# Kernel tuning notes

Hardware: AMD Instinct MI355X
Metric: run time of the kernel (lower is better)

Reference implementation:

```python
import jax, jax.numpy as jnp
import numpy as np

NUM_HEADS = 8
ROPE_THETA = 10.0


def _axial_angles(height, width, head_dim, theta):
    # frequencies: 1/theta^(arange(0, head_dim, 4)[:head_dim//4] / head_dim)  -> [head_dim//4]
    hd4 = head_dim // 4
    freqs = 1.0 / (theta ** (np.arange(0, head_dim, 4)[:hd4].astype(np.float32) / head_dim))
    t = np.arange(height * width)
    t_x = (t % width).astype(np.float32)
    t_y = (t // width).astype(np.float32)
    ang_x = np.outer(t_x, freqs)  # [n, head_dim//4]
    ang_y = np.outer(t_y, freqs)
    return jnp.asarray(ang_x), jnp.asarray(ang_y)


def _apply_rope(x, cos, sin):
    # x: [b, h, n, half]; cos/sin: [n, half//2]; complex-pair rotation on last dim
    xr = x[..., 0::2]
    xi = x[..., 1::2]
    out_r = xr * cos - xi * sin
    out_i = xr * sin + xi * cos
    return jnp.stack([out_r, out_i], axis=-1).reshape(x.shape)


def setup_inputs() -> dict:
    key = jax.random.key(0)
    ks = jax.random.split(key, 5)
    b, n, c = 4, 16384, 512
    x = jax.random.normal(ks[0], (b, n, c), dtype=jnp.float32)
    w_qkv = jax.random.normal(ks[1], (c, 3 * c), dtype=jnp.float32) * 0.02
    b_qkv = jax.random.normal(ks[2], (3 * c,), dtype=jnp.float32) * 0.02
    w_proj = jax.random.normal(ks[3], (c, c), dtype=jnp.float32) * 0.02
    b_proj = jax.random.normal(ks[4], (c,), dtype=jnp.float32) * 0.02
    return {"x": x, "w_qkv": w_qkv, "b_qkv": b_qkv, "w_proj": w_proj, "b_proj": b_proj,
            "height": 128, "width": 128}


def reference(x, w_qkv, b_qkv, w_proj, b_proj, height, width):
    b, n, c = x.shape
    h = NUM_HEADS
    hd = c // h
    half = hd // 2

    qkv = (x @ w_qkv + b_qkv).reshape(b, n, 3, h, hd).transpose(2, 0, 3, 1, 4)
    q, k, v = qkv[0], qkv[1], qkv[2]  # each [b, h, n, hd]

    ang_x, ang_y = _axial_angles(height, width, hd, ROPE_THETA)
    cx, sx = jnp.cos(ang_x), jnp.sin(ang_x)
    cy, sy = jnp.cos(ang_y), jnp.sin(ang_y)

    q = jnp.concatenate([_apply_rope(q[..., :half], cx, sx),
                         _apply_rope(q[..., half:], cy, sy)], axis=-1)
    k = jnp.concatenate([_apply_rope(k[..., :half], cx, sx),
                         _apply_rope(k[..., half:], cy, sy)], axis=-1)

    # kernel feature map: elu(x) + 1 (positive)
    q = jax.nn.elu(q) + 1.0
    k = jax.nn.elu(k) + 1.0

    # linear attention: O(n d^2)
    kv = jnp.einsum('bhnd,bhne->bhde', k, v)
    out = jnp.einsum('bhnd,bhde->bhne', q, kv)
    z = 1.0 / (jnp.einsum('bhnd,bhd->bhn', q, k.sum(axis=2)) + 1e-6)
    out = out * z[..., None]

    out = out.transpose(0, 2, 1, 3).reshape(b, n, c)
    return out @ w_proj + b_proj
```

## Files before the change

kernel.cpp:

```cpp
#include <hip/hip_runtime.h>
#include <math.h>

#define BATCH 4
#define NTOK  16384
#define CDIM  512
#define NH    8
#define HD    64
#define M_ROWS (BATCH*NTOK)
#define KDIM  512

typedef _Float16 f16;
typedef _Float16 f16x8 __attribute__((ext_vector_type(8)));
typedef _Float16 f16x4 __attribute__((ext_vector_type(4)));
typedef _Float16 f16x2 __attribute__((ext_vector_type(2)));
typedef float    f32x4 __attribute__((ext_vector_type(4)));

__device__ __forceinline__ void load_lds16(const void* g, void* l) {
    __builtin_amdgcn_global_load_lds(
        (const __attribute__((address_space(1))) void*)g,
        (__attribute__((address_space(3))) void*)l, 16, 0, 0);
}

__global__ void rope_tables(float* __restrict__ tab) {
    int tid = threadIdx.x;
    for (int i = 0; i < 32; i++) {
        int idx = tid + i * 256;
        int grp = idx >> 11;
        int rem = idx & 2047;
        int t   = rem >> 4;
        int fi  = rem & 15;
        float freq_f = (float)pow(10.0, -(double)fi / 16.0);
        double ang = (double)t * (double)freq_f;
        tab[idx] = (float)((grp & 1) ? sin(ang) : cos(ang));
    }
}

__global__ void convert_x_f16(const float* __restrict__ in, f16* __restrict__ outp) {
    int i = blockIdx.x * 256 + threadIdx.x;
    float4 a = *(const float4*)&in[(size_t)i * 8];
    float4 b = *(const float4*)&in[(size_t)i * 8 + 4];
    f16x8 o;
    o[0]=(f16)a.x; o[1]=(f16)a.y; o[2]=(f16)a.z; o[3]=(f16)a.w;
    o[4]=(f16)b.x; o[5]=(f16)b.y; o[6]=(f16)b.z; o[7]=(f16)b.w;
    *(f16x8*)&outp[(size_t)i * 8] = o;
}

__global__ void convert_wT(const float* __restrict__ w, f16* __restrict__ wt, int N) {
    int idx = blockIdx.x * 256 + threadIdx.x;
    int n = idx >> 9, k = idx & 511;
    wt[idx] = (f16)w[(size_t)k * N + n];
}

template<int MODE>
__global__ __launch_bounds__(256, 2)
void gemm_f16(const f16* __restrict__ A, const f16* __restrict__ Bt,
              const float* __restrict__ bias,
              float* __restrict__ Co,
              f16* __restrict__ qd, f16* __restrict__ kd, f16* __restrict__ vd,
              const float* __restrict__ tab)
{
    __shared__ f16 As[128 * 32];
    __shared__ f16 Bs[128 * 32];
    const int tid  = threadIdx.x;
    const int lane = tid & 63;
    const int wave = tid >> 6;
    const int wy = wave >> 1, wx = wave & 1;
    const int row0 = blockIdx.y * 128;
    const int col0 = blockIdx.x * 128;
    const int l15 = lane & 15;
    const int l4  = lane >> 4;

    f32x4 acc[4][4];
    #pragma unroll
    for (int mt = 0; mt < 4; mt++)
        #pragma unroll
        for (int nt = 0; nt < 4; nt++)
            acc[mt][nt] = (f32x4){0.f, 0.f, 0.f, 0.f};

    const int pbase = wave * 128;

    for (int k0 = 0; k0 < KDIM; k0 += 32) {
        #pragma unroll
        for (int i = 0; i < 2; i++) {
            int p = pbase + i * 64 + lane;
            int m = p >> 2;
            int j = p & 3;
            load_lds16(&A [(size_t)(row0 + m) * KDIM + k0 + j * 8], &As[(pbase + i * 64) * 8]);
            load_lds16(&Bt[(size_t)(col0 + m) * KDIM + k0 + j * 8], &Bs[(pbase + i * 64) * 8]);
        }
        __syncthreads();

        f16x8 af[4], bf[4];
        #pragma unroll
        for (int t = 0; t < 4; t++) {
            af[t] = *(const f16x8*)&As[(wy * 64 + t * 16 + l15) * 32 + l4 * 8];
            bf[t] = *(const f16x8*)&Bs[(wx * 64 + t * 16 + l15) * 32 + l4 * 8];
        }
        #pragma unroll
        for (int mt = 0; mt < 4; mt++)
            #pragma unroll
            for (int nt = 0; nt < 4; nt++)
                acc[mt][nt] = __builtin_amdgcn_mfma_f32_16x16x32_f16(af[mt], bf[nt], acc[mt][nt], 0, 0, 0);
        __syncthreads();
    }

    if (MODE == 0) {
        #pragma unroll
        for (int nt = 0; nt < 4; nt++) {
            int col = col0 + wx * 64 + nt * 16 + l15;
            float bv = bias[col];
            #pragma unroll
            for (int mt = 0; mt < 4; mt++)
                #pragma unroll
                for (int r = 0; r < 4; r++) {
                    int row = row0 + wy * 64 + mt * 16 + l4 * 4 + r;
                    Co[(size_t)row * CDIM + col] = acc[mt][nt][r] + bv;
                }
        }
    } else {
        const int which = col0 >> 9;
        f16* dst = (which == 0) ? qd : (which == 1) ? kd : vd;
        #pragma unroll
        for (int nt = 0; nt < 4; nt++) {
            int coln = col0 + wx * 64 + nt * 16 + l15;
            int c512 = coln & 511;
            float bv = bias[coln];
            if (which == 2) {
                #pragma unroll
                for (int mt = 0; mt < 4; mt++)
                    #pragma unroll
                    for (int r = 0; r < 4; r++) {
                        int row = row0 + wy * 64 + mt * 16 + l4 * 4 + r;
                        float val = acc[mt][nt][r] + bv;
                        float pv  = __shfl_xor(val, 1, 64);
                        if (!(lane & 1)) {
                            f16x2 pk; pk[0] = (f16)val; pk[1] = (f16)pv;
                            *(f16x2*)&dst[(size_t)row * CDIM + c512] = pk;
                        }
                    }
            } else {
                int ch  = c512 & 63;
                int isy = ch >> 5;
                int fid = (ch & 31) >> 1;
                const float* ct = tab + (isy ? 4096 : 0)    + fid;
                const float* st = tab + (isy ? 6144 : 2048) + fid;
                #pragma unroll
                for (int mt = 0; mt < 4; mt++)
                    #pragma unroll
                    for (int r = 0; r < 4; r++) {
                        int row = row0 + wy * 64 + mt * 16 + l4 * 4 + r;
                        int tok = row & (NTOK - 1);
                        int t   = isy ? (tok >> 7) : (tok & 127);
                        float c = ct[t * 16], s = st[t * 16];
                        float val = acc[mt][nt][r] + bv;
                        float pv  = __shfl_xor(val, 1, 64);
                        float xr = (lane & 1) ? pv  : val;
                        float xi = (lane & 1) ? val : pv;
                        float o_r = xr * c - xi * s;
                        float o_i = xr * s + xi * c;
                        o_r = (o_r > 0.f) ? o_r + 1.f : __expf(o_r);
                        o_i = (o_i > 0.f) ? o_i + 1.f : __expf(o_i);
                        if (!(lane & 1)) {
                            f16x2 pk; pk[0] = (f16)o_r; pk[1] = (f16)o_i;
                            *(f16x2*)&dst[(size_t)row * CDIM + c512] = pk;
                        }
                    }
            }
        }
    }
}

__global__ __launch_bounds__(256, 4)
void kv_kernel(const f16* __restrict__ kk, const f16* __restrict__ vv,
               float* __restrict__ kv, float* __restrict__ ksum)
{
    int bh = blockIdx.x;
    int b = bh >> 3, h = bh & 7;
    int t0 = blockIdx.y * 1024;
    __shared__ float ks[64][64];
    __shared__ float vs[64][64];
    int tid = threadIdx.x;
    int tx = tid & 15;
    int ty = tid >> 4;
    float acc[4][4];
    float ksacc[4];
    #pragma unroll
    for (int r = 0; r < 4; r++) { ksacc[r] = 0.f;
        #pragma unroll
        for (int j = 0; j < 4; j++) acc[r][j] = 0.f; }

    const size_t rowbase = (size_t)b * NTOK;
    for (int tt = t0; tt < t0 + 1024; tt += 64) {
        #pragma unroll
        for (int i = 0; i < 2; i++) {
            int idx = tid + i * 256;
            int tok = idx >> 3;
            int o   = (idx & 7) * 8;
            size_t g = (rowbase + tt + tok) * CDIM + h * HD + o;
            f16x8 k8 = *(const f16x8*)&kk[g];
            f16x8 v8 = *(const f16x8*)&vv[g];
            #pragma unroll
            for (int e = 0; e < 8; e++) { ks[tok][o + e] = (float)k8[e]; vs[tok][o + e] = (float)v8[e]; }
        }
        __syncthreads();
        #pragma unroll 8
        for (int t = 0; t < 64; t++) {
            float4 kd4 = *(const float4*)&ks[t][ty * 4];
            float4 vd4 = *(const float4*)&vs[t][tx * 4];
            float ka[4] = {kd4.x, kd4.y, kd4.z, kd4.w};
            float va[4] = {vd4.x, vd4.y, vd4.z, vd4.w};
            #pragma unroll
            for (int r = 0; r < 4; r++) {
                ksacc[r] += ka[r];
                #pragma unroll
                for (int j = 0; j < 4; j++) acc[r][j] += ka[r] * va[j];
            }
        }
        __syncthreads();
    }
    #pragma unroll
    for (int r = 0; r < 4; r++)
        #pragma unroll
        for (int j = 0; j < 4; j++)
            atomicAdd(&kv[bh * 4096 + (ty * 4 + r) * 64 + tx * 4 + j], acc[r][j]);
    if (tx == 0) {
        #pragma unroll
        for (int r = 0; r < 4; r++) atomicAdd(&ksum[bh * 64 + ty * 4 + r], ksacc[r]);
    }
}

__global__ __launch_bounds__(256, 4)
void attn_kernel(const f16* __restrict__ q, const float* __restrict__ kv,
                 const float* __restrict__ ksum, f16* __restrict__ attnh)
{
    int bh = blockIdx.x;
    int b = bh >> 3, h = bh & 7;
    int rc = blockIdx.y;
    __shared__ float kvs[64][64];
    __shared__ float qs[64][68];
    __shared__ float ksums[64];
    __shared__ float zpart[64][4];
    __shared__ float zs[64];
    int tid = threadIdx.x;
    int tx = tid & 15;
    int ty = tid >> 4;

    #pragma unroll
    for (int i = 0; i < 4; i++) {
        int idx = tid + i * 256;
        *(float4*)&kvs[idx >> 4][(idx & 15) * 4] = *(const float4*)&kv[bh * 4096 + idx * 4];
    }
    if (tid < 64) ksums[tid] = ksum[bh * 64 + tid];

    for (int sub = 0; sub < 4; sub++) {
        int r0 = rc * 256 + sub * 64;
        #pragma unroll
        for (int i = 0; i < 2; i++) {
            int idx = tid + i * 256;
            int rr = idx >> 3;
            int o  = (idx & 7) * 8;
            f16x8 q8 = *(const f16x8*)&q[((size_t)b * NTOK + r0 + rr) * CDIM + h * HD + o];
            #pragma unroll
            for (int e = 0; e < 8; e++) qs[rr][o + e] = (float)q8[e];
        }
        __syncthreads();
        {
            int row = tid & 63, g = tid >> 6;
            float p = 0.f;
            #pragma unroll
            for (int d = 0; d < 16; d++) p += qs[row][g * 16 + d] * ksums[g * 16 + d];
            zpart[row][g] = p;
        }
        __syncthreads();
        if (tid < 64)
            zs[tid] = 1.f / (zpart[tid][0] + zpart[tid][1] + zpart[tid][2] + zpart[tid][3] + 1e-6f);
        __syncthreads();

        float acc[4][4];
        #pragma unroll
        for (int r = 0; r < 4; r++)
            #pragma unroll
            for (int e = 0; e < 4; e++) acc[r][e] = 0.f;

        for (int d = 0; d < 64; d += 4) {
            float qa[4][4], ka[4][4];
            #pragma unroll
            for (int r = 0; r < 4; r++) {
                float4 v4 = *(const float4*)&qs[ty * 4 + r][d];
                qa[r][0]=v4.x; qa[r][1]=v4.y; qa[r][2]=v4.z; qa[r][3]=v4.w;
            }
            #pragma unroll
            for (int j = 0; j < 4; j++) {
                float4 v4 = *(const float4*)&kvs[d + j][tx * 4];
                ka[j][0]=v4.x; ka[j][1]=v4.y; ka[j][2]=v4.z; ka[j][3]=v4.w;
            }
            #pragma unroll
            for (int r = 0; r < 4; r++)
                #pragma unroll
                for (int j = 0; j < 4; j++)
                    #pragma unroll
                    for (int e = 0; e < 4; e++)
                        acc[r][e] += qa[r][j] * ka[j][e];
        }
        #pragma unroll
        for (int r = 0; r < 4; r++) {
            float z = zs[ty * 4 + r];
            f16x4 o4;
            o4[0] = (f16)(acc[r][0] * z); o4[1] = (f16)(acc[r][1] * z);
            o4[2] = (f16)(acc[r][2] * z); o4[3] = (f16)(acc[r][3] * z);
            *(f16x4*)&attnh[((size_t)b * NTOK + r0 + ty * 4 + r) * CDIM + h * HD + tx * 4] = o4;
        }
        __syncthreads();
    }
}

extern "C" void kernel_launch(void* const* d_in, const int* in_sizes, int n_in,
                              void* d_out, int out_size, void* d_ws, size_t ws_size,
                              hipStream_t stream)
{
    const float* x      = (const float*)d_in[0];
    const float* w_qkv  = (const float*)d_in[1];
    const float* b_qkv  = (const float*)d_in[2];
    const float* w_proj = (const float*)d_in[3];
    const float* b_proj = (const float*)d_in[4];
    float* out = (float*)d_out;
    char*  ws  = (char*)d_ws;

    const size_t NCB = (size_t)M_ROWS * CDIM * sizeof(f16);
    f16*   xh   = (f16*)(ws);
    f16*   qh   = (f16*)(ws + NCB * 1);
    f16*   kh   = (f16*)(ws + NCB * 2);
    f16*   vh   = (f16*)(ws + NCB * 3);
    f16*   wqt  = (f16*)(ws + NCB * 4);
    f16*   wpt  = (f16*)(ws + NCB * 4 + (1536 * 512) * sizeof(f16));
    float* tab  = (float*)(ws + NCB * 4 + (1536 * 512 + 512 * 512) * sizeof(f16));
    float* kvp  = tab + 8192;
    float* ksum = kvp + 32 * 4096;

    hipMemsetAsync(kvp, 0, (32 * 4096 + 32 * 64) * sizeof(float), stream);
    rope_tables<<<1, 256, 0, stream>>>(tab);
    convert_x_f16<<<M_ROWS * CDIM / 8 / 256, 256, 0, stream>>>(x, xh);
    convert_wT<<<1536 * 512 / 256, 256, 0, stream>>>(w_qkv, wqt, 1536);
    convert_wT<<<512 * 512 / 256, 256, 0, stream>>>(w_proj, wpt, 512);

    gemm_f16<1><<<dim3(12, 512), 256, 0, stream>>>(xh, wqt, b_qkv,
                                                   nullptr, qh, kh, vh, tab);
    kv_kernel<<<dim3(32, 16), 256, 0, stream>>>(kh, vh, kvp, ksum);
    attn_kernel<<<dim3(32, 64), 256, 0, stream>>>(qh, kvp, ksum, vh);
    gemm_f16<0><<<dim3(4, 512), 256, 0, stream>>>(vh, wpt, b_proj,
                                                  out, nullptr, nullptr, nullptr, nullptr);
}
```

Before: 671.2 us.

## Remap GEMM blocks per XCD, double K-step, stage epilogue via LDS, pad attention smem

The GEMM grid is flattened, and block IDs are remapped so that row tiles are grouped by XCD (bid&7). The aim is for the blocks sharing A rows to share an L2. The K loop now loads two 32-wide K slices per barrier pair, which halves the synchronisations. The MODE 0 epilogue stages results through LDS so that stores to global memory are coalesced float4 writes. The kv and attn kernels pad their LDS rows to 68 and write the converted values as float4 stores to reduce bank conflicts. These changes raise LDS usage and add barriers in the epilogue.

```diff
diff --git a/kernel.cpp b/kernel.cpp
--- a/kernel.cpp
+++ b/kernel.cpp
@@ -57,16 +57,23 @@
               const float* __restrict__ bias,
               float* __restrict__ Co,
               f16* __restrict__ qd, f16* __restrict__ kd, f16* __restrict__ vd,
-              const float* __restrict__ tab)
+              const float* __restrict__ tab, int ncol_tiles)
 {
-    __shared__ f16 As[128 * 32];
-    __shared__ f16 Bs[128 * 32];
+    __shared__ f16 As[2][128 * 32];
+    __shared__ f16 Bs[2][128 * 32];
     const int tid  = threadIdx.x;
     const int lane = tid & 63;
     const int wave = tid >> 6;
     const int wy = wave >> 1, wx = wave & 1;
-    const int row0 = blockIdx.y * 128;
-    const int col0 = blockIdx.x * 128;
+
+    const int bid = blockIdx.x;
+    const int xcd = bid & 7;
+    const int idx = bid >> 3;
+    const int ct  = idx % ncol_tiles;
+    const int rt  = (idx / ncol_tiles) * 8 + xcd;
+    const int row0 = rt * 128;
+    const int col0 = ct * 128;
+
     const int l15 = lane & 15;
     const int l4  = lane >> 4;
 
@@ -79,43 +86,62 @@
 
     const int pbase = wave * 128;
 
-    for (int k0 = 0; k0 < KDIM; k0 += 32) {
-        #pragma unroll
-        for (int i = 0; i < 2; i++) {
-            int p = pbase + i * 64 + lane;
-            int m = p >> 2;
-            int j = p & 3;
-            load_lds16(&A [(size_t)(row0 + m) * KDIM + k0 + j * 8], &As[(pbase + i * 64) * 8]);
-            load_lds16(&Bt[(size_t)(col0 + m) * KDIM + k0 + j * 8], &Bs[(pbase + i * 64) * 8]);
-        }
-        __syncthreads();
-
-        f16x8 af[4], bf[4];
-        #pragma unroll
-        for (int t = 0; t < 4; t++) {
-            af[t] = *(const f16x8*)&As[(wy * 64 + t * 16 + l15) * 32 + l4 * 8];
-            bf[t] = *(const f16x8*)&Bs[(wx * 64 + t * 16 + l15) * 32 + l4 * 8];
-        }
-        #pragma unroll
-        for (int mt = 0; mt < 4; mt++)
-            #pragma unroll
-            for (int nt = 0; nt < 4; nt++)
-                acc[mt][nt] = __builtin_amdgcn_mfma_f32_16x16x32_f16(af[mt], bf[nt], acc[mt][nt], 0, 0, 0);
+    for (int k0 = 0; k0 < KDIM; k0 += 64) {
+        #pragma unroll
+        for (int s = 0; s < 2; s++)
+            #pragma unroll
+            for (int i = 0; i < 2; i++) {
+                int p = pbase + i * 64 + lane;
+                int m = p >> 2;
+                int j = p & 3;
+                load_lds16(&A [(size_t)(row0 + m) * KDIM + k0 + s * 32 + j * 8],
+                           &As[s][(pbase + i * 64) * 8]);
+                load_lds16(&Bt[(size_t)(col0 + m) * KDIM + k0 + s * 32 + j * 8],
+                           &Bs[s][(pbase + i * 64) * 8]);
+            }
+        __syncthreads();
+
+        #pragma unroll
+        for (int s = 0; s < 2; s++) {
+            f16x8 af[4], bf[4];
+            #pragma unroll
+            for (int t = 0; t < 4; t++) {
+                af[t] = *(const f16x8*)&As[s][(wy * 64 + t * 16 + l15) * 32 + l4 * 8];
+                bf[t] = *(const f16x8*)&Bs[s][(wx * 64 + t * 16 + l15) * 32 + l4 * 8];
+            }
+            #pragma unroll
+            for (int mt = 0; mt < 4; mt++)
+                #pragma unroll
+                for (int nt = 0; nt < 4; nt++)
+                    acc[mt][nt] = __builtin_amdgcn_mfma_f32_16x16x32_f16(af[mt], bf[nt], acc[mt][nt], 0, 0, 0);
+        }
         __syncthreads();
     }
 
     if (MODE == 0) {
-        #pragma unroll
-        for (int nt = 0; nt < 4; nt++) {
-            int col = col0 + wx * 64 + nt * 16 + l15;
-            float bv = bias[col];
-            #pragma unroll
-            for (int mt = 0; mt < 4; mt++)
+        float* ep = (float*)&As[0][0];
+        #pragma unroll
+        for (int mt = 0; mt < 4; mt++) {
+            #pragma unroll
+            for (int nt = 0; nt < 4; nt++) {
+                int col = wx * 64 + nt * 16 + l15;
+                float bv = bias[col0 + col];
                 #pragma unroll
                 for (int r = 0; r < 4; r++) {
-                    int row = row0 + wy * 64 + mt * 16 + l4 * 4 + r;
-                    Co[(size_t)row * CDIM + col] = acc[mt][nt][r] + bv;
+                    int rp = wy * 16 + l4 * 4 + r;
+                    ep[rp * 128 + col] = acc[mt][nt][r] + bv;
                 }
+            }
+            __syncthreads();
+            #pragma unroll
+            for (int j = 0; j < 4; j++) {
+                int id = tid + j * 256;
+                int rp = id >> 5, c4 = id & 31;
+                int grow = row0 + (rp >> 4) * 64 + mt * 16 + (rp & 15);
+                float4 v4 = *(const float4*)&ep[rp * 128 + c4 * 4];
+                *(float4*)&Co[(size_t)grow * CDIM + col0 + c4 * 4] = v4;
+            }
+            __syncthreads();
         }
     } else {
         const int which = col0 >> 9;
@@ -142,8 +168,8 @@
                 int ch  = c512 & 63;
                 int isy = ch >> 5;
                 int fid = (ch & 31) >> 1;
-                const float* ct = tab + (isy ? 4096 : 0)    + fid;
-                const float* st = tab + (isy ? 6144 : 2048) + fid;
+                const float* ctb = tab + (isy ? 4096 : 0)    + fid;
+                const float* stb = tab + (isy ? 6144 : 2048) + fid;
                 #pragma unroll
                 for (int mt = 0; mt < 4; mt++)
                     #pragma unroll
@@ -151,7 +177,7 @@
                         int row = row0 + wy * 64 + mt * 16 + l4 * 4 + r;
                         int tok = row & (NTOK - 1);
                         int t   = isy ? (tok >> 7) : (tok & 127);
-                        float c = ct[t * 16], s = st[t * 16];
+                        float c = ctb[t * 16], s = stb[t * 16];
                         float val = acc[mt][nt][r] + bv;
                         float pv  = __shfl_xor(val, 1, 64);
                         float xr = (lane & 1) ? pv  : val;
@@ -177,8 +203,8 @@
     int bh = blockIdx.x;
     int b = bh >> 3, h = bh & 7;
     int t0 = blockIdx.y * 1024;
-    __shared__ float ks[64][64];
-    __shared__ float vs[64][64];
+    __shared__ float ks[64][68];
+    __shared__ float vs[64][68];
     int tid = threadIdx.x;
     int tx = tid & 15;
     int ty = tid >> 4;
@@ -199,8 +225,14 @@
             size_t g = (rowbase + tt + tok) * CDIM + h * HD + o;
             f16x8 k8 = *(const f16x8*)&kk[g];
             f16x8 v8 = *(const f16x8*)&vv[g];
-            #pragma unroll
-            for (int e = 0; e < 8; e++) { ks[tok][o + e] = (float)k8[e]; vs[tok][o + e] = (float)v8[e]; }
+            float4 klo = {(float)k8[0], (float)k8[1], (float)k8[2], (float)k8[3]};
+            float4 khi = {(float)k8[4], (float)k8[5], (float)k8[6], (float)k8[7]};
+            float4 vlo = {(float)v8[0], (float)v8[1], (float)v8[2], (float)v8[3]};
+            float4 vhi = {(float)v8[4], (float)v8[5], (float)v8[6], (float)v8[7]};
+            *(float4*)&ks[tok][o]     = klo;
+            *(float4*)&ks[tok][o + 4] = khi;
+            *(float4*)&vs[tok][o]     = vlo;
+            *(float4*)&vs[tok][o + 4] = vhi;
         }
         __syncthreads();
         #pragma unroll 8
@@ -236,7 +268,7 @@
     int bh = blockIdx.x;
     int b = bh >> 3, h = bh & 7;
     int rc = blockIdx.y;
-    __shared__ float kvs[64][64];
+    __shared__ float kvs[64][68];
     __shared__ float qs[64][68];
     __shared__ float ksums[64];
     __shared__ float zpart[64][4];
@@ -260,8 +292,10 @@
             int rr = idx >> 3;
             int o  = (idx & 7) * 8;
             f16x8 q8 = *(const f16x8*)&q[((size_t)b * NTOK + r0 + rr) * CDIM + h * HD + o];
-            #pragma unroll
-            for (int e = 0; e < 8; e++) qs[rr][o + e] = (float)q8[e];
+            float4 lo = {(float)q8[0], (float)q8[1], (float)q8[2], (float)q8[3]};
+            float4 hi = {(float)q8[4], (float)q8[5], (float)q8[6], (float)q8[7]};
+            *(float4*)&qs[rr][o]     = lo;
+            *(float4*)&qs[rr][o + 4] = hi;
         }
         __syncthreads();
         {
@@ -343,10 +377,10 @@
     convert_wT<<<1536 * 512 / 256, 256, 0, stream>>>(w_qkv, wqt, 1536);
     convert_wT<<<512 * 512 / 256, 256, 0, stream>>>(w_proj, wpt, 512);
 
-    gemm_f16<1><<<dim3(12, 512), 256, 0, stream>>>(xh, wqt, b_qkv,
-                                                   nullptr, qh, kh, vh, tab);
+    gemm_f16<1><<<6144, 256, 0, stream>>>(xh, wqt, b_qkv,
+                                          nullptr, qh, kh, vh, tab, 12);
     kv_kernel<<<dim3(32, 16), 256, 0, stream>>>(kh, vh, kvp, ksum);
     attn_kernel<<<dim3(32, 64), 256, 0, stream>>>(qh, kvp, ksum, vh);
-    gemm_f16<0><<<dim3(4, 512), 256, 0, stream>>>(vh, wpt, b_proj,
-                                                  out, nullptr, nullptr, nullptr, nullptr);
-}
+    gemm_f16<0><<<2048, 256, 0, stream>>>(vh, wpt, b_proj,
+                                          out, nullptr, nullptr, nullptr, nullptr, 4);
+}
```

After: 657.8 us. 1.02x faster.
